# Performance work log

Hardware: AMD Instinct MI355X
Metric: run time of the kernel (lower is better)

## Reference

```python
import jax, jax.numpy as jnp
import numpy as np

B, S, D, H = 2, 2048, 1024, 16
DK = D // H  # 64
THETA = 10000.0


def setup_inputs() -> dict:
    key = jax.random.key(0)
    ks = jax.random.split(key, 5)
    sigma = (2.0 / (D + DK)) ** 0.5
    return {
        "x": jax.random.normal(ks[0], (B, S, D), jnp.float32),
        "Wq": jax.random.normal(ks[1], (D, H * DK), jnp.float32) * sigma,
        "Wk": jax.random.normal(ks[2], (D, H * DK), jnp.float32) * sigma,
        "Wv": jax.random.normal(ks[3], (D, H * DK), jnp.float32) * sigma,
        "Wo": jax.random.normal(ks[4], (D, H * DK), jnp.float32) * sigma,
        "token_positions": jnp.arange(S, dtype=jnp.int32),
    }


def _rope(x, pos):
    # x: (B, H, S, DK); pos: (S,). Block-diag 2x2 rotation == paired rotation.
    half = DK // 2
    k = jnp.arange(half, dtype=jnp.float32)
    inv_freq = 1.0 / (THETA ** (2.0 * k / DK))          # (half,)
    ang = pos.astype(jnp.float32)[:, None] * inv_freq    # (S, half)
    cos, sin = jnp.cos(ang), jnp.sin(ang)
    xr = x.reshape(*x.shape[:-1], half, 2)
    x0, x1 = xr[..., 0], xr[..., 1]
    o0 = x0 * cos - x1 * sin
    o1 = x0 * sin + x1 * cos
    return jnp.stack([o0, o1], axis=-1).reshape(x.shape)


def reference(x, Wq, Wk, Wv, Wo, token_positions):
    # projections: einsum('... d_in, hd d_in -> ... hd') == x @ W.T
    def proj(W):
        return (x @ W.T).reshape(B, S, H, DK).transpose(0, 2, 1, 3)  # (B,H,S,DK)

    q, k, v = proj(Wq), proj(Wk), proj(Wv)
    q = _rope(q, token_positions)
    k = _rope(k, token_positions)

    scores = jnp.einsum("bhqd,bhkd->bhqk", q, k) / jnp.sqrt(jnp.float32(DK))
    causal = jnp.tril(jnp.ones((S, S), bool))  # (S,S), True where attended
    scores = jnp.where(causal[None, None], scores, -jnp.inf)
    probs = jax.nn.softmax(scores, axis=-1)

    o = jnp.einsum("bhqk,bhkd->bhqd", probs, v)
    o = o.transpose(0, 2, 1, 3).reshape(B, S, H * DK)
    return o @ Wo.T  # einsum('... d_out, d_model d_out -> ... d_model')
```

## Files before the change

kernel.cpp:

```cpp
#include <hip/hip_runtime.h>

typedef __bf16 bf16;
typedef __bf16 bf16x4 __attribute__((ext_vector_type(4)));
typedef __bf16 bf16x8 __attribute__((ext_vector_type(8)));
typedef float f32x4 __attribute__((ext_vector_type(4)));

#define MFMA16(a, b, c) __builtin_amdgcn_mfma_f32_16x16x32_bf16((a), (b), (c), 0, 0, 0)

constexpr int B_ = 2, S_ = 2048, D_ = 1024, H_ = 16, DK_ = 64;

__device__ __forceinline__ void gload16(const bf16* g, bf16* l)
{
  __builtin_amdgcn_global_load_lds(
      (const __attribute__((address_space(1))) uint32_t*)g,
      (__attribute__((address_space(3))) uint32_t*)l, 16, 0, 0);
}

__global__ __launch_bounds__(256) void cvt_k(
    const float* __restrict__ x, const float* __restrict__ Wq, const float* __restrict__ Wk,
    const float* __restrict__ Wv, const float* __restrict__ Wo, bf16* __restrict__ ws)
{
  size_t f = ((size_t)blockIdx.x * 256 + threadIdx.x) * 4;
  const float* src;
  bf16* dst;
  size_t off;
  if (f < 4194304) {
    src = x; dst = ws; off = f;
  } else {
    size_t g = f - 4194304;
    int wsel = (int)(g >> 20);
    off = g & 1048575;
    src = wsel == 0 ? Wq : wsel == 1 ? Wk : wsel == 2 ? Wv : Wo;
    dst = ws + 4194304 + ((size_t)wsel << 20);
  }
  float4 v = *(const float4*)(src + off);
  bf16x4 o = {(bf16)v.x, (bf16)v.y, (bf16)v.z, (bf16)v.w};
  *(bf16x4*)(dst + off) = o;
}

template <typename TY, int PERM>
__global__ __launch_bounds__(256) void gemm_k(
    const bf16* __restrict__ A,
    const bf16* __restrict__ W0, const bf16* __restrict__ W1, const bf16* __restrict__ W2,
    TY* __restrict__ Y0, TY* __restrict__ Y1, TY* __restrict__ Y2,
    int Kdim, float scale0)
{
  __shared__ __align__(16) bf16 As[128 * 64];
  __shared__ __align__(16) bf16 Bs[128 * 64];
  const int t = threadIdx.x, l = t & 63, w = t >> 6;
  const int wm = w >> 1, wn = w & 1;
  const int m0 = blockIdx.x * 128, n0 = blockIdx.y * 128;
  const int z = blockIdx.z;
  const bf16* W = z == 0 ? W0 : z == 1 ? W1 : W2;
  TY* Y = z == 0 ? Y0 : z == 1 ? Y1 : Y2;
  const float scale = (PERM == 1 && z == 0) ? scale0 : 1.0f;

  f32x4 acc[4][4] = {};

  for (int k0 = 0; k0 < Kdim; k0 += 64) {
    __syncthreads();
#pragma unroll
    for (int j = 0; j < 4; ++j) {
      int slot = j * 256 + t;
      int row = slot >> 3, c8 = slot & 7;
      int csw = (c8 ^ (row & 7)) << 3;
      gload16(A + (size_t)(m0 + row) * Kdim + k0 + csw, &As[(j * 256 + w * 64) * 8]);
      gload16(W + (size_t)(n0 + row) * Kdim + k0 + csw, &Bs[(j * 256 + w * 64) * 8]);
    }
    asm volatile("s_waitcnt vmcnt(0)" ::: "memory");
    __syncthreads();
#pragma unroll
    for (int kk = 0; kk < 2; ++kk) {
      bf16x8 af[4], bfr[4];
#pragma unroll
      for (int i = 0; i < 4; ++i) {
        int Ra = wm * 64 + i * 16 + (l & 15);
        int Rb = wn * 64 + i * 16 + (l & 15);
        int c = kk * 4 + (l >> 4);
        af[i] = *(const bf16x8*)&As[Ra * 64 + ((c ^ (Ra & 7)) << 3)];
        bfr[i] = *(const bf16x8*)&Bs[Rb * 64 + ((c ^ (Rb & 7)) << 3)];
      }
#pragma unroll
      for (int mi = 0; mi < 4; ++mi)
#pragma unroll
        for (int ni = 0; ni < 4; ++ni)
          acc[mi][ni] = MFMA16(af[mi], bfr[ni], acc[mi][ni]);
    }
  }

#pragma unroll
  for (int mi = 0; mi < 4; ++mi)
#pragma unroll
    for (int ni = 0; ni < 4; ++ni)
#pragma unroll
      for (int j = 0; j < 4; ++j) {
        int m = m0 + wm * 64 + mi * 16 + (l >> 4) * 4 + j;
        int n = n0 + wn * 64 + ni * 16 + (l & 15);
        float v = acc[mi][ni][j] * scale;
        if (PERM == 0) {
          Y[(size_t)m * 1024 + n] = (TY)v;
        } else {
          int b = m >> 11, s = m & (S_ - 1), h = n >> 6, d = n & (DK_ - 1);
          Y[(((size_t)(b * H_ + h)) * S_ + s) * DK_ + d] = (TY)v;
        }
      }
}

__global__ __launch_bounds__(256) void rope_k(
    bf16* __restrict__ Q, bf16* __restrict__ K, const int* __restrict__ pos)
{
  int i = blockIdx.x * 256 + threadIdx.x;
  bf16* buf = (i < 262144) ? Q : K;
  int idx = i & 262143;
  int kpg = idx & 3;
  int s = (idx >> 2) & (S_ - 1);
  int bh = idx >> 13;
  float p = (float)pos[s];
  size_t off = ((size_t)bh * S_ + s) * DK_ + kpg * 16;
  bf16x8 lo = *(const bf16x8*)(buf + off);
  bf16x8 hi = *(const bf16x8*)(buf + off + 8);
  bf16x8 olo, ohi;
#pragma unroll
  for (int ii = 0; ii < 8; ++ii) {
    int kp = kpg * 8 + ii;
    float ang = p * exp2f((float)kp * -0.41524101186017f);
    float sn, cs;
    __sincosf(ang, &sn, &cs);
    float x0 = (float)((ii < 4 ? lo : hi)[(ii & 3) * 2]);
    float x1 = (float)((ii < 4 ? lo : hi)[(ii & 3) * 2 + 1]);
    bf16 o0 = (bf16)(x0 * cs - x1 * sn);
    bf16 o1 = (bf16)(x0 * sn + x1 * cs);
    if (ii < 4) { olo[(ii & 3) * 2] = o0; olo[(ii & 3) * 2 + 1] = o1; }
    else        { ohi[(ii & 3) * 2] = o0; ohi[(ii & 3) * 2 + 1] = o1; }
  }
  *(bf16x8*)(buf + off) = olo;
  *(bf16x8*)(buf + off + 8) = ohi;
}

__device__ __forceinline__ void qk_mfma(const bf16* Kbuf, int l, bf16x8 aq0, bf16x8 aq1,
                                        f32x4 sc4[4])
{
#pragma unroll
  for (int nf = 0; nf < 4; ++nf) {
    int R = nf * 16 + (l & 15);
    int c0 = l >> 4;
    bf16x8 b0 = *(const bf16x8*)&Kbuf[R * 64 + ((c0 ^ (R & 7)) << 3)];
    bf16x8 b1 = *(const bf16x8*)&Kbuf[R * 64 + (((4 + c0) ^ (R & 7)) << 3)];
    f32x4 s = {};
    s = MFMA16(aq0, b0, s);
    s = MFMA16(aq1, b1, s);
    sc4[nf] = s;
  }
}

__device__ __forceinline__ void diag_mask(int w, int l, f32x4 sc4[4])
{
#pragma unroll
  for (int nf = 0; nf < 4; ++nf)
#pragma unroll
    for (int j = 0; j < 4; ++j) {
      int kvl = nf * 16 + (l & 15);
      int ql = w * 16 + (l >> 4) * 4 + j;
      if (kvl > ql) sc4[nf][j] = -1e30f;
    }
}

__device__ __forceinline__ void tile_update(
    int l, const f32x4 sc4[4], f32x4 acc[4], float mrun[4], float lsum[4],
    bf16 (*Pw)[72], const bf16 (*Vc)[72])
{
  float pm[4];
#pragma unroll
  for (int j = 0; j < 4; ++j)
    pm[j] = fmaxf(fmaxf(sc4[0][j], sc4[1][j]), fmaxf(sc4[2][j], sc4[3][j]));
#pragma unroll
  for (int m = 1; m <= 8; m <<= 1)
#pragma unroll
    for (int j = 0; j < 4; ++j)
      pm[j] = fmaxf(pm[j], __shfl_xor(pm[j], m, 64));

  float alpha[4];
#pragma unroll
  for (int j = 0; j < 4; ++j) {
    float nm = fmaxf(mrun[j], pm[j]);
    alpha[j] = exp2f(mrun[j] - nm);
    mrun[j] = nm;
  }

  float rs[4] = {0.f, 0.f, 0.f, 0.f};
#pragma unroll
  for (int nf = 0; nf < 4; ++nf)
#pragma unroll
    for (int j = 0; j < 4; ++j) {
      float p = exp2f(sc4[nf][j] - mrun[j]);
      rs[j] += p;
      Pw[(l >> 4) * 4 + j][nf * 16 + (l & 15)] = (bf16)p;
    }
#pragma unroll
  for (int m = 1; m <= 8; m <<= 1)
#pragma unroll
    for (int j = 0; j < 4; ++j)
      rs[j] += __shfl_xor(rs[j], m, 64);
#pragma unroll
  for (int j = 0; j < 4; ++j) lsum[j] = lsum[j] * alpha[j] + rs[j];
#pragma unroll
  for (int nf = 0; nf < 4; ++nf)
#pragma unroll
    for (int j = 0; j < 4; ++j)
      acc[nf][j] *= alpha[j];

  asm volatile("s_waitcnt lgkmcnt(0)" ::: "memory");

  __builtin_amdgcn_s_setprio(1);
#pragma unroll
  for (int kk = 0; kk < 2; ++kk) {
    bf16x8 ap = *(const bf16x8*)&Pw[l & 15][kk * 32 + (l >> 4) * 8];
#pragma unroll
    for (int nf = 0; nf < 4; ++nf) {
      bf16x8 bv = *(const bf16x8*)&Vc[nf * 16 + (l & 15)][kk * 32 + (l >> 4) * 8];
      acc[nf] = MFMA16(ap, bv, acc[nf]);
    }
  }
  __builtin_amdgcn_s_setprio(0);
}

__global__ __launch_bounds__(256, 3) void attn_k(
    const bf16* __restrict__ Q, const bf16* __restrict__ K, const bf16* __restrict__ V,
    bf16* __restrict__ O)
{
  __shared__ __align__(16) bf16 Klds[2][64 * 64];
  __shared__ __align__(16) bf16 Vt[2][64][72];
  __shared__ __align__(16) bf16 PsA[4][16][72];
  __shared__ __align__(16) bf16 PsB[4][16][72];

  const int t = threadIdx.x, l = t & 63, w = t >> 6;
  const int bh = blockIdx.x >> 4;
  const int qp = blockIdx.x & 15;
  const int qtB = (bh & 16) ? (15 - qp) : qp;
  const int qtA = 31 - qtB;
  const int b = bh >> 4, h = bh & 15;
  const size_t base = (size_t)bh * S_ * DK_;
  const int q0A = qtA * 64, q0B = qtB * 64;

  const int qrow = w * 16 + (l & 15), qcol = (l >> 4) * 8;
  const bf16* pqA = Q + base + (size_t)(q0A + qrow) * 64 + qcol;
  const bf16* pqB = Q + base + (size_t)(q0B + qrow) * 64 + qcol;
  bf16x8 aqA0 = *(const bf16x8*)pqA, aqA1 = *(const bf16x8*)(pqA + 32);
  bf16x8 aqB0 = *(const bf16x8*)pqB, aqB1 = *(const bf16x8*)(pqB + 32);

  {
#pragma unroll
    for (int j = 0; j < 2; ++j) {
      int slot = j * 256 + t, row = slot >> 3, c8 = slot & 7;
      gload16(K + base + (size_t)row * 64 + ((c8 ^ (row & 7)) << 3),
              &Klds[0][(j * 256 + w * 64) * 8]);
    }
    const bf16* pv = V + base + (size_t)l * 64 + w * 16;
    bf16x8 v0 = *(const bf16x8*)pv, v1 = *(const bf16x8*)(pv + 8);
    asm volatile("s_waitcnt vmcnt(0)" ::: "memory");
#pragma unroll
    for (int i = 0; i < 8; ++i) {
      Vt[0][w * 16 + i][l] = v0[i];
      Vt[0][w * 16 + 8 + i][l] = v1[i];
    }
  }
  __syncthreads();

  f32x4 accA[4] = {}, accB[4] = {};
  float mrunA[4], lsumA[4], mrunB[4], lsumB[4];
#pragma unroll
  for (int j = 0; j < 4; ++j) {
    mrunA[j] = mrunB[j] = -1e30f;
    lsumA[j] = lsumB[j] = 0.f;
  }

  int cur = 0;
  for (int tk = 0; tk <= qtA; ++tk) {
    const int nxt = cur ^ 1;
    const bool hasn = tk < qtA;
    bf16x8 v0, v1;
    if (hasn) {
      const int kv0n = (tk + 1) * 64;
#pragma unroll
      for (int j = 0; j < 2; ++j) {
        int slot = j * 256 + t, row = slot >> 3, c8 = slot & 7;
        gload16(K + base + (size_t)(kv0n + row) * 64 + ((c8 ^ (row & 7)) << 3),
                &Klds[nxt][(j * 256 + w * 64) * 8]);
      }
      const bf16* pv = V + base + (size_t)(kv0n + l) * 64 + w * 16;
      v0 = *(const bf16x8*)pv;
      v1 = *(const bf16x8*)(pv + 8);
    }

    const bool actB = tk <= qtB;
    f32x4 scA[4], scB[4];
    __builtin_amdgcn_s_setprio(1);
    qk_mfma(Klds[cur], l, aqA0, aqA1, scA);
    if (actB) qk_mfma(Klds[cur], l, aqB0, aqB1, scB);
    __builtin_amdgcn_s_setprio(0);
    if (tk == qtA) diag_mask(w, l, scA);
    if (actB && tk == qtB) diag_mask(w, l, scB);

    tile_update(l, scA, accA, mrunA, lsumA, PsA[w], Vt[cur]);
    if (actB) tile_update(l, scB, accB, mrunB, lsumB, PsB[w], Vt[cur]);

    if (hasn) {
      asm volatile("s_waitcnt vmcnt(0)" ::: "memory");
#pragma unroll
      for (int i = 0; i < 8; ++i) {
        Vt[nxt][w * 16 + i][l] = v0[i];
        Vt[nxt][w * 16 + 8 + i][l] = v1[i];
      }
    }
    __syncthreads();
    cur = nxt;
  }

#pragma unroll
  for (int nf = 0; nf < 4; ++nf)
#pragma unroll
    for (int j = 0; j < 4; ++j) {
      int r = w * 16 + (l >> 4) * 4 + j;
      int d = nf * 16 + (l & 15);
      O[((size_t)(b * S_ + q0A + r) * H_ + h) * DK_ + d] = (bf16)(accA[nf][j] / lsumA[j]);
      O[((size_t)(b * S_ + q0B + r) * H_ + h) * DK_ + d] = (bf16)(accB[nf][j] / lsumB[j]);
    }
}

extern "C" void kernel_launch(void* const* d_in, const int* in_sizes, int n_in,
                              void* d_out, int out_size, void* d_ws, size_t ws_size,
                              hipStream_t stream)
{
  const float* x = (const float*)d_in[0];
  const float* Wq = (const float*)d_in[1];
  const float* Wk = (const float*)d_in[2];
  const float* Wv = (const float*)d_in[3];
  const float* Wo = (const float*)d_in[4];
  const int* pos = (const int*)d_in[5];

  bf16* ws = (bf16*)d_ws;
  const size_t NE = (size_t)B_ * H_ * S_ * DK_;
  bf16* xb = ws;
  bf16* Wqb = ws + NE;
  bf16* Wkb = Wqb + 1048576;
  bf16* Wvb = Wkb + 1048576;
  bf16* Wob = Wvb + 1048576;
  bf16* Qb = Wob + 1048576;
  bf16* Kb = Qb + NE;
  bf16* Vb = Kb + NE;
  bf16* Ob = xb;

  dim3 blk(256);

  hipLaunchKernelGGL(cvt_k, dim3(8192), blk, 0, stream, x, Wq, Wk, Wv, Wo, ws);

  hipLaunchKernelGGL((gemm_k<bf16, 1>), dim3(32, 8, 3), blk, 0, stream,
                     xb, Wqb, Wkb, Wvb, Qb, Kb, Vb, 1024, 0.125f * 1.4426950408889634f);

  hipLaunchKernelGGL(rope_k, dim3(2048), blk, 0, stream, Qb, Kb, pos);

  hipLaunchKernelGGL(attn_k, dim3(32 * 16), blk, 0, stream, Qb, Kb, Vb, Ob);

  hipLaunchKernelGGL((gemm_k<float, 0>), dim3(32, 8, 1), blk, 0, stream,
                     Ob, Wob, Wob, Wob, (float*)d_out, (float*)d_out, (float*)d_out,
                     1024, 1.0f);
}
```

Measured before the change: 155.2 us.

## Split paired-Q attention blocks into single-tile blocks with lazy rescale and swizzled LDS

The attention kernel now processes one 64-row query tile per block instead of a paired long/short pair, doubling the grid to 1024 blocks. Blocks are ordered with a heavy/light interleave so the causal triangle stays balanced, and launch bounds rise to 4 waves per SIMD. V^T and P tiles move to an XOR-swizzled unpadded layout to cut LDS bank conflicts and footprint. Online-softmax rescaling is skipped when the new row max stays within a threshold of the running max. The trade-off is that each K/V tile is now loaded once per query tile instead of being shared by two, which doubles K/V traffic.

```diff
diff --git a/kernel.cpp b/kernel.cpp
--- a/kernel.cpp
+++ b/kernel.cpp
@@ -137,116 +137,27 @@
   *(bf16x8*)(buf + off + 8) = ohi;
 }
 
-__device__ __forceinline__ void qk_mfma(const bf16* Kbuf, int l, bf16x8 aq0, bf16x8 aq1,
-                                        f32x4 sc4[4])
-{
-#pragma unroll
-  for (int nf = 0; nf < 4; ++nf) {
-    int R = nf * 16 + (l & 15);
-    int c0 = l >> 4;
-    bf16x8 b0 = *(const bf16x8*)&Kbuf[R * 64 + ((c0 ^ (R & 7)) << 3)];
-    bf16x8 b1 = *(const bf16x8*)&Kbuf[R * 64 + (((4 + c0) ^ (R & 7)) << 3)];
-    f32x4 s = {};
-    s = MFMA16(aq0, b0, s);
-    s = MFMA16(aq1, b1, s);
-    sc4[nf] = s;
-  }
-}
-
-__device__ __forceinline__ void diag_mask(int w, int l, f32x4 sc4[4])
-{
-#pragma unroll
-  for (int nf = 0; nf < 4; ++nf)
-#pragma unroll
-    for (int j = 0; j < 4; ++j) {
-      int kvl = nf * 16 + (l & 15);
-      int ql = w * 16 + (l >> 4) * 4 + j;
-      if (kvl > ql) sc4[nf][j] = -1e30f;
-    }
-}
-
-__device__ __forceinline__ void tile_update(
-    int l, const f32x4 sc4[4], f32x4 acc[4], float mrun[4], float lsum[4],
-    bf16 (*Pw)[72], const bf16 (*Vc)[72])
-{
-  float pm[4];
-#pragma unroll
-  for (int j = 0; j < 4; ++j)
-    pm[j] = fmaxf(fmaxf(sc4[0][j], sc4[1][j]), fmaxf(sc4[2][j], sc4[3][j]));
-#pragma unroll
-  for (int m = 1; m <= 8; m <<= 1)
-#pragma unroll
-    for (int j = 0; j < 4; ++j)
-      pm[j] = fmaxf(pm[j], __shfl_xor(pm[j], m, 64));
-
-  float alpha[4];
-#pragma unroll
-  for (int j = 0; j < 4; ++j) {
-    float nm = fmaxf(mrun[j], pm[j]);
-    alpha[j] = exp2f(mrun[j] - nm);
-    mrun[j] = nm;
-  }
-
-  float rs[4] = {0.f, 0.f, 0.f, 0.f};
-#pragma unroll
-  for (int nf = 0; nf < 4; ++nf)
-#pragma unroll
-    for (int j = 0; j < 4; ++j) {
-      float p = exp2f(sc4[nf][j] - mrun[j]);
-      rs[j] += p;
-      Pw[(l >> 4) * 4 + j][nf * 16 + (l & 15)] = (bf16)p;
-    }
-#pragma unroll
-  for (int m = 1; m <= 8; m <<= 1)
-#pragma unroll
-    for (int j = 0; j < 4; ++j)
-      rs[j] += __shfl_xor(rs[j], m, 64);
-#pragma unroll
-  for (int j = 0; j < 4; ++j) lsum[j] = lsum[j] * alpha[j] + rs[j];
-#pragma unroll
-  for (int nf = 0; nf < 4; ++nf)
-#pragma unroll
-    for (int j = 0; j < 4; ++j)
-      acc[nf][j] *= alpha[j];
-
-  asm volatile("s_waitcnt lgkmcnt(0)" ::: "memory");
-
-  __builtin_amdgcn_s_setprio(1);
-#pragma unroll
-  for (int kk = 0; kk < 2; ++kk) {
-    bf16x8 ap = *(const bf16x8*)&Pw[l & 15][kk * 32 + (l >> 4) * 8];
-#pragma unroll
-    for (int nf = 0; nf < 4; ++nf) {
-      bf16x8 bv = *(const bf16x8*)&Vc[nf * 16 + (l & 15)][kk * 32 + (l >> 4) * 8];
-      acc[nf] = MFMA16(ap, bv, acc[nf]);
-    }
-  }
-  __builtin_amdgcn_s_setprio(0);
-}
-
-__global__ __launch_bounds__(256, 3) void attn_k(
+__global__ __launch_bounds__(256, 4) void attn_k(
     const bf16* __restrict__ Q, const bf16* __restrict__ K, const bf16* __restrict__ V,
     bf16* __restrict__ O)
 {
   __shared__ __align__(16) bf16 Klds[2][64 * 64];
-  __shared__ __align__(16) bf16 Vt[2][64][72];
-  __shared__ __align__(16) bf16 PsA[4][16][72];
-  __shared__ __align__(16) bf16 PsB[4][16][72];
+  __shared__ __align__(16) bf16 Vt[2][64 * 64];
+  __shared__ __align__(16) bf16 Ps[4][16 * 64];
 
   const int t = threadIdx.x, l = t & 63, w = t >> 6;
-  const int bh = blockIdx.x >> 4;
-  const int qp = blockIdx.x & 15;
-  const int qtB = (bh & 16) ? (15 - qp) : qp;
-  const int qtA = 31 - qtB;
+  const int bx = blockIdx.x;
+  const int i5 = bx >> 5;
+  const int bh = bx & 31;
+  const int a = i5 & 7, bq = i5 >> 3;
+  const int qt = (bq == 0) ? (31 - a) : (bq == 1) ? a : (bq == 2) ? (16 + a) : (15 - a);
   const int b = bh >> 4, h = bh & 15;
   const size_t base = (size_t)bh * S_ * DK_;
-  const int q0A = qtA * 64, q0B = qtB * 64;
+  const int q0 = qt * 64;
 
   const int qrow = w * 16 + (l & 15), qcol = (l >> 4) * 8;
-  const bf16* pqA = Q + base + (size_t)(q0A + qrow) * 64 + qcol;
-  const bf16* pqB = Q + base + (size_t)(q0B + qrow) * 64 + qcol;
-  bf16x8 aqA0 = *(const bf16x8*)pqA, aqA1 = *(const bf16x8*)(pqA + 32);
-  bf16x8 aqB0 = *(const bf16x8*)pqB, aqB1 = *(const bf16x8*)(pqB + 32);
+  const bf16* pq = Q + base + (size_t)(q0 + qrow) * 64 + qcol;
+  bf16x8 aq0 = *(const bf16x8*)pq, aq1 = *(const bf16x8*)(pq + 32);
 
   {
 #pragma unroll
@@ -259,25 +170,23 @@
     bf16x8 v0 = *(const bf16x8*)pv, v1 = *(const bf16x8*)(pv + 8);
     asm volatile("s_waitcnt vmcnt(0)" ::: "memory");
 #pragma unroll
-    for (int i = 0; i < 8; ++i) {
-      Vt[0][w * 16 + i][l] = v0[i];
-      Vt[0][w * 16 + 8 + i][l] = v1[i];
+    for (int ii = 0; ii < 8; ++ii) {
+      int d0 = w * 16 + ii, d1 = w * 16 + 8 + ii;
+      Vt[0][d0 * 64 + (((l >> 3) ^ (d0 & 7)) << 3) + (l & 7)] = v0[ii];
+      Vt[0][d1 * 64 + (((l >> 3) ^ (d1 & 7)) << 3) + (l & 7)] = v1[ii];
     }
   }
   __syncthreads();
 
-  f32x4 accA[4] = {}, accB[4] = {};
-  float mrunA[4], lsumA[4], mrunB[4], lsumB[4];
-#pragma unroll
-  for (int j = 0; j < 4; ++j) {
-    mrunA[j] = mrunB[j] = -1e30f;
-    lsumA[j] = lsumB[j] = 0.f;
-  }
+  f32x4 acc[4] = {};
+  float mrun[4], lsum[4];
+#pragma unroll
+  for (int j = 0; j < 4; ++j) { mrun[j] = -1e30f; lsum[j] = 0.f; }
 
   int cur = 0;
-  for (int tk = 0; tk <= qtA; ++tk) {
+  for (int tk = 0; tk <= qt; ++tk) {
     const int nxt = cur ^ 1;
-    const bool hasn = tk < qtA;
+    const bool hasn = tk < qt;
     bf16x8 v0, v1;
     if (hasn) {
       const int kv0n = (tk + 1) * 64;
@@ -292,25 +201,102 @@
       v1 = *(const bf16x8*)(pv + 8);
     }
 
-    const bool actB = tk <= qtB;
-    f32x4 scA[4], scB[4];
+    f32x4 sc[4];
     __builtin_amdgcn_s_setprio(1);
-    qk_mfma(Klds[cur], l, aqA0, aqA1, scA);
-    if (actB) qk_mfma(Klds[cur], l, aqB0, aqB1, scB);
+#pragma unroll
+    for (int nf = 0; nf < 4; ++nf) {
+      int R = nf * 16 + (l & 15);
+      int c0 = l >> 4;
+      bf16x8 b0 = *(const bf16x8*)&Klds[cur][R * 64 + ((c0 ^ (R & 7)) << 3)];
+      bf16x8 b1 = *(const bf16x8*)&Klds[cur][R * 64 + (((4 + c0) ^ (R & 7)) << 3)];
+      f32x4 s = {};
+      s = MFMA16(aq0, b0, s);
+      s = MFMA16(aq1, b1, s);
+      sc[nf] = s;
+    }
     __builtin_amdgcn_s_setprio(0);
-    if (tk == qtA) diag_mask(w, l, scA);
-    if (actB && tk == qtB) diag_mask(w, l, scB);
-
-    tile_update(l, scA, accA, mrunA, lsumA, PsA[w], Vt[cur]);
-    if (actB) tile_update(l, scB, accB, mrunB, lsumB, PsB[w], Vt[cur]);
+
+    if (tk == qt) {
+#pragma unroll
+      for (int nf = 0; nf < 4; ++nf)
+#pragma unroll
+        for (int j = 0; j < 4; ++j) {
+          int kvl = nf * 16 + (l & 15);
+          int ql = w * 16 + (l >> 4) * 4 + j;
+          if (kvl > ql) sc[nf][j] = -1e30f;
+        }
+    }
+
+    {
+      float pm[4];
+#pragma unroll
+      for (int j = 0; j < 4; ++j)
+        pm[j] = fmaxf(fmaxf(sc[0][j], sc[1][j]), fmaxf(sc[2][j], sc[3][j]));
+#pragma unroll
+      for (int m = 1; m <= 8; m <<= 1)
+#pragma unroll
+        for (int j = 0; j < 4; ++j)
+          pm[j] = fmaxf(pm[j], __shfl_xor(pm[j], m, 64));
+
+      bool defer = true;
+#pragma unroll
+      for (int j = 0; j < 4; ++j) defer = defer && (pm[j] <= mrun[j] + 11.0f);
+      if (!__all(defer)) {
+#pragma unroll
+        for (int j = 0; j < 4; ++j) {
+          float nm = fmaxf(mrun[j], pm[j]);
+          float al = exp2f(mrun[j] - nm);
+          mrun[j] = nm;
+          lsum[j] *= al;
+#pragma unroll
+          for (int nf = 0; nf < 4; ++nf) acc[nf][j] *= al;
+        }
+      }
+
+      float rs[4] = {0.f, 0.f, 0.f, 0.f};
+#pragma unroll
+      for (int nf = 0; nf < 4; ++nf)
+#pragma unroll
+        for (int j = 0; j < 4; ++j) {
+          float p = exp2f(sc[nf][j] - mrun[j]);
+          rs[j] += p;
+          int r = (l >> 4) * 4 + j, c = nf * 16 + (l & 15);
+          Ps[w][r * 64 + ((((c >> 3) ^ (r & 7))) << 3) + (c & 7)] = (bf16)p;
+        }
+#pragma unroll
+      for (int m = 1; m <= 8; m <<= 1)
+#pragma unroll
+        for (int j = 0; j < 4; ++j)
+          rs[j] += __shfl_xor(rs[j], m, 64);
+#pragma unroll
+      for (int j = 0; j < 4; ++j) lsum[j] += rs[j];
+    }
+
+    asm volatile("s_waitcnt lgkmcnt(0)" ::: "memory");
+
+    __builtin_amdgcn_s_setprio(1);
+#pragma unroll
+    for (int kk = 0; kk < 2; ++kk) {
+      int rp = l & 15;
+      int c8p = kk * 4 + (l >> 4);
+      bf16x8 ap = *(const bf16x8*)&Ps[w][rp * 64 + ((c8p ^ (rp & 7)) << 3)];
+#pragma unroll
+      for (int nf = 0; nf < 4; ++nf) {
+        int R = nf * 16 + (l & 15);
+        bf16x8 bv = *(const bf16x8*)&Vt[cur][R * 64 + ((c8p ^ (R & 7)) << 3)];
+        acc[nf] = MFMA16(ap, bv, acc[nf]);
+      }
+    }
+    __builtin_amdgcn_s_setprio(0);
 
     if (hasn) {
+#pragma unroll
+      for (int ii = 0; ii < 8; ++ii) {
+        int d0 = w * 16 + ii, d1 = w * 16 + 8 + ii;
+        Vt[nxt][d0 * 64 + (((l >> 3) ^ (d0 & 7)) << 3) + (l & 7)] = v0[ii];
+        Vt[nxt][d1 * 64 + (((l >> 3) ^ (d1 & 7)) << 3) + (l & 7)] = v1[ii];
+      }
       asm volatile("s_waitcnt vmcnt(0)" ::: "memory");
-#pragma unroll
-      for (int i = 0; i < 8; ++i) {
-        Vt[nxt][w * 16 + i][l] = v0[i];
-        Vt[nxt][w * 16 + 8 + i][l] = v1[i];
-      }
     }
     __syncthreads();
     cur = nxt;
@@ -322,8 +308,7 @@
     for (int j = 0; j < 4; ++j) {
       int r = w * 16 + (l >> 4) * 4 + j;
       int d = nf * 16 + (l & 15);
-      O[((size_t)(b * S_ + q0A + r) * H_ + h) * DK_ + d] = (bf16)(accA[nf][j] / lsumA[j]);
-      O[((size_t)(b * S_ + q0B + r) * H_ + h) * DK_ + d] = (bf16)(accB[nf][j] / lsumB[j]);
+      O[((size_t)(b * S_ + q0 + r) * H_ + h) * DK_ + d] = (bf16)(acc[nf][j] / lsum[j]);
     }
 }
 
@@ -359,7 +344,7 @@
 
   hipLaunchKernelGGL(rope_k, dim3(2048), blk, 0, stream, Qb, Kb, pos);
 
-  hipLaunchKernelGGL(attn_k, dim3(32 * 16), blk, 0, stream, Qb, Kb, Vb, Ob);
+  hipLaunchKernelGGL(attn_k, dim3(1024), blk, 0, stream, Qb, Kb, Vb, Ob);
 
   hipLaunchKernelGGL((gemm_k<float, 0>), dim3(32, 8, 1), blk, 0, stream,
                      Ob, Wob, Wob, Wob, (float*)d_out, (float*)d_out, (float*)d_out,
```

Measured after the change: 147.7 us. -4.8%, faster.
